# Optimization experiments

Measured on AMD Instinct MI355X. Metric: run time of the kernel, lower is better.

The kernel has to match this reference:

```python
import jax, jax.numpy as jnp
from jax import lax
import numpy as np

# ---- hyperparams (match init_kwargs) ----
NUM_HASHES = 8
BITS = 5
TABLE_SIZE = 64
M = 27            # ALSH augmentation length; M % (KH*KW) == 0
U = 0.83
KH = KW = 3
STRIDE = 1
PAD = 1
OUT_CHANNELS = 256
IN_CHANNELS = 64


def setup_inputs() -> dict:
    key = jax.random.key(0)
    k1, k2, k3 = jax.random.split(key, 3)
    x = jax.random.normal(k1, (32, IN_CHANNELS, 56, 56), jnp.float32)
    kernels = jax.random.normal(k2, (OUT_CHANNELS, IN_CHANNELS, KH, KW), jnp.float32) * 0.05
    a = jax.random.normal(k3, (NUM_HASHES * BITS, IN_CHANNELS * KH * KW + M), jnp.float32)
    return {"x": x, "kernels": kernels, "a": a}


def _scale_under_U(kv):
    # ScaleUnder_U: rescale all kernel vectors so max L2 norm == U
    norms = jnp.sqrt(jnp.sum(kv * kv, axis=1))
    return kv * (U / jnp.max(norms))


def _P(kv):
    # ALSH preprocessing: append ||x||^2, ||x||^4, ..., ||x||^(2^M)
    p = jnp.sum(kv * kv, axis=1, keepdims=True)  # ||x||^2
    cols = []
    for _ in range(M):
        cols.append(p)
        p = p * p
    return jnp.concatenate([kv] + cols, axis=1)  # [K, D+M]


_BIT_W = (2 ** jnp.arange(BITS)).astype(jnp.int32)


def _hash_vectors(a, v):
    # v: [K, D+M] -> bucket indices [NUM_HASHES, K]
    proj = v @ a.T                                   # [K, NUM_HASHES*BITS]
    bits = (proj > 0).astype(jnp.int32).reshape(-1, NUM_HASHES, BITS)
    idx = jnp.einsum('khb,b->hk', bits, _BIT_W)      # multi-bit SRP index
    return idx % TABLE_SIZE


def _build_table(bucket):
    # vectorized equivalent of the nested scalar-scatter loops in init_table:
    # append kernel id i to table[bucket[h, i]] in (h-major, i-minor) order.
    H, K = bucket.shape
    flat = bucket.reshape(-1)                        # [H*K]
    vals = (jnp.arange(H * K) % K).astype(jnp.int32) # stored value = kernel index i
    order = jnp.argsort(flat)                        # stable in jax
    sb, sv = flat[order], vals[order]
    pos = jnp.arange(H * K) - jnp.searchsorted(sb, sb, side='left')  # slot within bucket
    row_len = H * K
    table = jnp.zeros((TABLE_SIZE, row_len), jnp.int32).at[sb, pos].set(sv)
    lengths = jnp.zeros((TABLE_SIZE,), jnp.int32).at[flat].add(1)
    return table, lengths


def _vote_buckets(x, a):
    # Q: append M/(KH*KW) constant 1/2 planes; hash via convolution with a reshaped
    N, C, H, W = x.shape
    m_planes = M // (KH * KW)
    xq = jnp.concatenate([x, jnp.full((N, m_planes, H, W), 0.5, x.dtype)], axis=1)
    hk = a.reshape(NUM_HASHES * BITS, C + m_planes, KH, KW)  # a_to_kernel
    d = lax.conv_general_dilated(xq, hk, (STRIDE, STRIDE), [(PAD, PAD), (PAD, PAD)],
                                 dimension_numbers=('NCHW', 'OIHW', 'NCHW'))
    # [N, NUM_HASHES*BITS, H', W'] -> bucket per (hash fn, location)
    Np, _, Hp, Wp = d.shape
    bits = (d > 0).astype(jnp.int32).reshape(Np, NUM_HASHES, BITS, Hp * Wp)
    buckets = jnp.einsum('nhbs,b->hns', bits, _BIT_W) % TABLE_SIZE  # [H, N, S]
    return buckets.reshape(NUM_HASHES, -1)


def _active_mask(x, kernels, a):
    K = kernels.shape[0]
    kv = kernels.reshape(K, -1)
    buckets_k = _hash_vectors(a, _P(_scale_under_U(kv)))   # [H, K]
    table, lengths = _build_table(buckets_k)
    votes = _vote_buckets(x, a)                            # [H, N*S]
    tallied = jnp.zeros((NUM_HASHES, TABLE_SIZE), jnp.int32).at[
        jnp.arange(NUM_HASHES)[:, None], votes].add(1)     # count_votes
    indices = jnp.argmax(tallied, axis=1)                  # best bucket per hash fn
    entries = table[indices]                               # [H, row_len]
    valid = jnp.arange(table.shape[1])[None, :] < lengths[indices][:, None]
    # union of kernel ids across selected buckets (== sort+unique gather)
    mask = jnp.zeros((K,), jnp.float32).at[entries.reshape(-1)].max(
        valid.reshape(-1).astype(jnp.float32))
    return mask, tallied, indices


def reference(x, kernels, a):
    mask, tallied, indices = _active_mask(x, kernels, a)
    out = lax.conv_general_dilated(x, kernels, (STRIDE, STRIDE), [(PAD, PAD), (PAD, PAD)],
                                   dimension_numbers=('NCHW', 'OIHW', 'NCHW'))
    out = out * mask[None, :, None, None]  # conv restricted to the active kernel set
    return out, tallied, indices, mask
```

## Files before the change

### kernel.cpp

```cpp
#include <hip/hip_runtime.h>
#include <math.h>

#define NH 8
#define BITS_ 5
#define NB 40
#define TS 64
#define MAUG 27
#define CIN 64
#define HH 56
#define WW 56
#define NN 32
#define OCH 256
#define DK 576
#define DPM 603
#define HW (HH*WW)

#define UST 59
#define LO_OFF 7552
#define SMEM_DW 15104

typedef __attribute__((ext_vector_type(4))) float f32x4;
typedef __attribute__((ext_vector_type(8))) _Float16 f16x8;
typedef union { uint4 u; f16x8 h; } fragh_u;

__device__ __forceinline__ unsigned int f16b(float v) {
    union { _Float16 h; unsigned short u; } cv;
    cv.h = (_Float16)v;
    return (unsigned int)cv.u;
}
__device__ __forceinline__ float f16tof(unsigned int b) {
    union { _Float16 h; unsigned short u; } cv;
    cv.u = (unsigned short)b;
    return (float)cv.h;
}

__global__ void kP(const float* __restrict__ kern, const float* __restrict__ a,
                   float* __restrict__ aT, float* __restrict__ ctab,
                   int* __restrict__ tallied, float* __restrict__ normP,
                   unsigned short* __restrict__ whA,
                   unsigned short* __restrict__ vaH, unsigned short* __restrict__ vaL)
{
    const int bid = blockIdx.x;
    const int t = threadIdx.x;
    if (bid < 32) {
        for (int idx = bid * 256 + t; idx < DPM * NB; idx += 32 * 256) {
            int d = idx / NB, j = idx - d * NB;
            aT[idx] = a[j * DPM + d];
        }
    } else if (bid == 32) {
        for (int g = t; g < 9 * NB; g += 256) {
            int pat = g / NB, j = g - pat * NB;
            int ry = pat / 3, rx = pat % 3;
            float s = 0.f;
            for (int ky = 0; ky < 3; ++ky) {
                if (ry == 0 && ky == 0) continue;
                if (ry == 2 && ky == 2) continue;
                for (int kx = 0; kx < 3; ++kx) {
                    if (rx == 0 && kx == 0) continue;
                    if (rx == 2 && kx == 2) continue;
                    for (int mc = 0; mc < 3; ++mc)
                        s += a[j * DPM + DK + mc * 9 + ky * 3 + kx];
                }
            }
            ctab[g] = 0.5f * s;
        }
        for (int g = t; g < NH * TS; g += 256) tallied[g] = 0;
    } else if (bid < 37) {
        int g = (bid - 33) * 256 + t;
        int oc = g >> 2, part = g & 3;
        const float4* p = (const float4*)(kern + oc * DK + part * 144);
        float sq = 0.f;
        #pragma unroll 4
        for (int i = 0; i < 36; ++i) {
            float4 v = p[i];
            sq += v.x * v.x + v.y * v.y + v.z * v.z + v.w * v.w;
        }
        normP[g] = sq;
    } else {
        int idx = (bid - 37) * 256 + t;
        int f = idx >> 6, lane = idx & 63;
        if (f < 288) {
            const int kidxG = f >> 4, mf = f & 15;
            const int tap = kidxG % 9, cc = kidxG / 9;
            const int oc = mf * 16 + (lane & 15);
            const int cbase = cc * 32 + (lane >> 4) * 8;
            unsigned int hs[8];
            #pragma unroll
            for (int j = 0; j < 8; ++j)
                hs[j] = f16b(kern[oc * DK + (cbase + j) * 9 + tap]);
            unsigned int* p = (unsigned int*)(whA + ((size_t)f * 64 + lane) * 8);
            #pragma unroll
            for (int w2 = 0; w2 < 4; ++w2)
                p[w2] = hs[2 * w2] | (hs[2 * w2 + 1] << 16);
        } else if (f < 342) {
            const int fv = f - 288;
            const int kidxG = fv / 3, mfv = fv % 3;
            const int tap = kidxG % 9, cc = kidxG / 9;
            const int j = mfv * 16 + (lane & 15);
            const int cbase = cc * 32 + (lane >> 4) * 8;
            unsigned int hs[8], ls[8];
            #pragma unroll
            for (int jj = 0; jj < 8; ++jj) {
                float w = (j < NB) ? a[j * DPM + (cbase + jj) * 9 + tap] : 0.f;
                unsigned int h = f16b(w);
                unsigned int l = f16b(w - f16tof(h));
                hs[jj] = h; ls[jj] = l;
            }
            unsigned int* ph = (unsigned int*)(vaH + ((size_t)fv * 64 + lane) * 8);
            unsigned int* pl = (unsigned int*)(vaL + ((size_t)fv * 64 + lane) * 8);
            #pragma unroll
            for (int w2 = 0; w2 < 4; ++w2) {
                ph[w2] = hs[2 * w2] | (hs[2 * w2 + 1] << 16);
                pl[w2] = ls[2 * w2] | (ls[2 * w2 + 1] << 16);
            }
        }
    }
}

__global__ void __launch_bounds__(256) kH(const float* __restrict__ kern,
        const float* __restrict__ aT, const float* __restrict__ normP,
        int* __restrict__ bucket_k)
{
    __shared__ float xs[DK];
    __shared__ float red[256];
    __shared__ float accR[3 * 41];
    __shared__ float proj[NB];
    const int t = threadIdx.x;
    const int lane = t & 63, ty = t >> 6;
    const int oc = blockIdx.x;

    red[t] = fmaxf(fmaxf(normP[t], normP[t + 256]), fmaxf(normP[t + 512], normP[t + 768]));
    __syncthreads();
    for (int s = 128; s > 0; s >>= 1) {
        if (t < s) red[t] = fmaxf(red[t], red[t + s]);
        __syncthreads();
    }
    const float scale = 0.83f / sqrtf(red[0]);
    for (int i = t; i < DK; i += 256) xs[i] = scale * kern[(size_t)oc * DK + i];
    __syncthreads();

    const int j = (lane < NB) ? lane : (NB - 1);
    float acc = 0.f, sq = 0.f;
    const int d0 = ty * 144;
    for (int d = d0; d < d0 + 144; ++d) {
        float xv = xs[d];
        sq += xv * xv;
        acc += xv * aT[d * NB + j];
    }
    if (ty > 0) {
        if (lane < NB) accR[(ty - 1) * 41 + lane] = acc;
        if (lane == NB) accR[(ty - 1) * 41 + 40] = sq;
    }
    __syncthreads();
    if (ty == 0 && lane < NB) {
        acc += (accR[lane] + accR[41 + lane]) + accR[82 + lane];
        sq += (accR[40] + accR[81]) + accR[122];
        float pv = sq;
        for (int m = 0; m < MAUG; ++m) {
            acc += pv * aT[(DK + m) * NB + lane];
            pv = pv * pv;
        }
        proj[lane] = acc;
    }
    __syncthreads();
    if (t < NH) {
        int b = 0;
        #pragma unroll
        for (int bb = 0; bb < BITS_; ++bb)
            if (proj[t * BITS_ + bb] > 0.f) b |= (1 << bb);
        bucket_k[t * OCH + oc] = b & (TS - 1);
    }
}

#define ADX(kidx, nb) ((rowu + ((((kidx) % 9) / 3) * 8 + ((kidx) / 9) * 4) * UST + (nb) + (((kidx) % 9) % 3)) * 4)

__global__ void __launch_bounds__(512, 4) kM(const float* __restrict__ x,
        const unsigned short* __restrict__ whA,
        const unsigned short* __restrict__ vaH, const unsigned short* __restrict__ vaL,
        const float* __restrict__ ctab, int* __restrict__ tallied,
        float* __restrict__ out)
{
    __shared__ unsigned int smem[SMEM_DW];
    const int lane = threadIdx.x, wid = threadIdx.y;
    const int y0 = blockIdx.x * 2, n = blockIdx.y;
    const int lcol = lane & 15, hi4 = lane >> 4;
    const int t = wid * 64 + lane;
    const int mg = wid & 3, ng = wid >> 2;
    const int colbase = (mg == 3) ? 40 : mg * 16;
    const uint4* wbase = (const uint4*)whA + (size_t)mg * 4 * 64 + lane;
    const int rowu = (ng * 8 + hi4) * UST + lcol;

    fragh_u ahA[4], ahB[4];
    #pragma unroll
    for (int mf = 0; mf < 4; ++mf) ahA[mf].u = wbase[mf * 64];

    {
        const int r = wid & 3, half = wid >> 2;
        const int y = y0 - 1 + r;
        const bool valid = (lane < WW) && (y >= 0) && (y < HH);
        const int colc = (lane < WW) ? lane : (WW - 1);
        const int yc = (y >= 0 && y < HH) ? y : 0;
        const float* xb = x + (((size_t)n * CIN + half * 32) * HH + yc) * WW + colc;
        float xv[32];
        #pragma unroll
        for (int i = 0; i < 32; ++i) xv[i] = xb[(size_t)i * HW];

        if (t < 256) {
            const int tile = t >> 7, rem = t & 127;
            const int L = (rem & 1) ? 57 : 0;
            const int u = (rem >> 1) & 7, rr = rem >> 4;
            *(uint4*)&smem[tile * LO_OFF + ((rr * 8 + u) * UST + L) * 4] =
                make_uint4(0u, 0u, 0u, 0u);
        }

        #pragma unroll
        for (int uu = 0; uu < 4; ++uu) {
            unsigned int dh[4], dl[4];
            #pragma unroll
            for (int dd = 0; dd < 4; ++dd) {
                float v0 = valid ? xv[uu * 8 + dd * 2] : 0.f;
                float v1 = valid ? xv[uu * 8 + dd * 2 + 1] : 0.f;
                unsigned int h0 = f16b(v0), h1 = f16b(v1);
                unsigned int l0 = f16b(v0 - f16tof(h0));
                unsigned int l1 = f16b(v1 - f16tof(h1));
                dh[dd] = h0 | (h1 << 16);
                dl[dd] = l0 | (l1 << 16);
            }
            if (lane < WW) {
                const int ad = ((r * 8 + half * 4 + uu) * UST + 1 + lane) * 4;
                *(uint4*)&smem[ad] = make_uint4(dh[0], dh[1], dh[2], dh[3]);
                *(uint4*)&smem[LO_OFF + ad] = make_uint4(dl[0], dl[1], dl[2], dl[3]);
            }
        }
    }
    __syncthreads();

    {
        f32x4 acc[4][4];
        #pragma unroll
        for (int mf = 0; mf < 4; ++mf)
            #pragma unroll
            for (int nf = 0; nf < 4; ++nf)
                acc[mf][nf] = (f32x4){0.f, 0.f, 0.f, 0.f};

        fragh_u bhP[3];
        bhP[0].u = *(const uint4*)&smem[ADX(0, 0)];
        bhP[1].u = *(const uint4*)&smem[ADX(0, 16)];

        #pragma unroll
        for (int step = 0; step < 72; ++step) {
            const int kidx = step >> 2, nf = step & 3;
            fragh_u* cur = (kidx & 1) ? ahB : ahA;
            fragh_u* nxt = (kidx & 1) ? ahA : ahB;
            if (nf == 0 && kidx < 17) {
                #pragma unroll
                for (int mf = 0; mf < 4; ++mf)
                    nxt[mf].u = wbase[(kidx + 1) * 1024 + mf * 64];
            }
            if (step + 2 < 72) {
                const int s2 = step + 2;
                const int k2 = s2 >> 2, nf2 = s2 & 3;
                const int nb2 = (nf2 == 3) ? 40 : nf2 * 16;
                bhP[s2 % 3].u = *(const uint4*)&smem[ADX(k2, nb2)];
            }
            const fragh_u bh = bhP[step % 3];
            acc[0][nf] = __builtin_amdgcn_mfma_f32_16x16x32_f16(cur[0].h, bh.h, acc[0][nf], 0, 0, 0);
            acc[1][nf] = __builtin_amdgcn_mfma_f32_16x16x32_f16(cur[1].h, bh.h, acc[1][nf], 0, 0, 0);
            acc[2][nf] = __builtin_amdgcn_mfma_f32_16x16x32_f16(cur[2].h, bh.h, acc[2][nf], 0, 0, 0);
            acc[3][nf] = __builtin_amdgcn_mfma_f32_16x16x32_f16(cur[3].h, bh.h, acc[3][nf], 0, 0, 0);
        }

        const int yrow = y0 + ng;
        #pragma unroll
        for (int mf = 0; mf < 4; ++mf) {
            #pragma unroll
            for (int reg = 0; reg < 4; ++reg) {
                const int oc = (mg * 4 + mf) * 16 + hi4 * 4 + reg;
                float* ob = out + (((size_t)n * OCH + oc) * HH + yrow) * WW;
                #pragma unroll
                for (int nf = 0; nf < 4; ++nf) {
                    const int col = ((nf == 3) ? 40 : nf * 16) + lcol;
                    ob[col] = acc[mf][nf][reg];
                }
            }
        }
    }

    f32x4 vacc[3];
    vacc[0] = (f32x4){0.f, 0.f, 0.f, 0.f};
    vacc[1] = (f32x4){0.f, 0.f, 0.f, 0.f};
    vacc[2] = (f32x4){0.f, 0.f, 0.f, 0.f};
    {
        const uint4* vbH = (const uint4*)vaH + lane;
        const uint4* vbL = (const uint4*)vaL + lane;
        fragh_u vh[3], vl[3];
        fragh_u bhV[2], blV[2];
        vh[0].u = vbH[0];   vl[0].u = vbL[0];
        vh[1].u = vbH[64];  vl[1].u = vbL[64];
        bhV[0].u = *(const uint4*)&smem[ADX(0, colbase)];
        blV[0].u = *(const uint4*)&smem[LO_OFF + ADX(0, colbase)];
        #pragma unroll
        for (int s = 0; s < 54; ++s) {
            const int kidx = s / 3, mfv = s % 3;
            const int b = kidx & 1;
            if (s + 2 < 54) {
                vh[(s + 2) % 3].u = vbH[(s + 2) * 64];
                vl[(s + 2) % 3].u = vbL[(s + 2) * 64];
            }
            if (mfv == 0 && kidx < 17) {
                bhV[b ^ 1].u = *(const uint4*)&smem[ADX(kidx + 1, colbase)];
                blV[b ^ 1].u = *(const uint4*)&smem[LO_OFF + ADX(kidx + 1, colbase)];
            }
            const fragh_u vhc = vh[s % 3], vlc = vl[s % 3];
            vacc[mfv] = __builtin_amdgcn_mfma_f32_16x16x32_f16(vhc.h, bhV[b].h, vacc[mfv], 0, 0, 0);
            vacc[mfv] = __builtin_amdgcn_mfma_f32_16x16x32_f16(vhc.h, blV[b].h, vacc[mfv], 0, 0, 0);
            vacc[mfv] = __builtin_amdgcn_mfma_f32_16x16x32_f16(vlc.h, bhV[b].h, vacc[mfv], 0, 0, 0);
        }
    }

    __syncthreads();
    float* projT = (float*)smem;
    int* hist = (int*)&smem[6144];
    {
        const int px = colbase + lcol;
        #pragma unroll
        for (int mfv = 0; mfv < 3; ++mfv)
            #pragma unroll
            for (int reg = 0; reg < 4; ++reg)
                projT[(ng * 64 + px) * 49 + mfv * 16 + hi4 * 4 + reg] = vacc[mfv][reg];
    }
    hist[t] = 0;
    __syncthreads();
    if (t < 2 * WW) {
        const int row = t / WW, pxx = t - row * WW;
        const int yv = y0 + row;
        const int ry = (yv == 0) ? 0 : ((yv == HH - 1) ? 2 : 1);
        const int rx = (pxx == 0) ? 0 : ((pxx == WW - 1) ? 2 : 1);
        const float* ct = ctab + (ry * 3 + rx) * NB;
        const float* pr = projT + (row * 64 + pxx) * 49;
        #pragma unroll
        for (int h = 0; h < NH; ++h) {
            int b = 0;
            #pragma unroll
            for (int bb = 0; bb < BITS_; ++bb)
                if (pr[h * BITS_ + bb] + ct[h * BITS_ + bb] > 0.f) b |= (1 << bb);
            atomicAdd(&hist[h * TS + (b & (TS - 1))], 1);
        }
    }
    __syncthreads();
    {
        int v = hist[t];
        if (v) atomicAdd(&tallied[t], v);
    }
}

__global__ void kC(const int* __restrict__ tallied, const int* __restrict__ bucket_k,
                   float* __restrict__ o_tallied, float* __restrict__ o_indices,
                   float* __restrict__ o_mask, int* __restrict__ mask_i)
{
    const int t = threadIdx.x;
    __shared__ int s_idx[NH];
    if (t < NH) {
        int best = tallied[t * TS];
        int bi = 0;
        for (int b = 1; b < TS; ++b) {
            int v = tallied[t * TS + b];
            if (v > best) { best = v; bi = b; }
        }
        s_idx[t] = bi;
        o_indices[t] = (float)bi;
    }
    for (int i = t; i < NH * TS; i += 256) o_tallied[i] = (float)tallied[i];
    __syncthreads();
    int mk = 0;
    #pragma unroll
    for (int hp = 0; hp < NH; ++hp) {
        int b = bucket_k[hp * OCH + t];
        #pragma unroll
        for (int h = 0; h < NH; ++h) mk |= (b == s_idx[h]) ? 1 : 0;
    }
    mask_i[t] = mk;
    o_mask[t] = (float)mk;
}

__global__ void __launch_bounds__(256) kZ(float* __restrict__ out,
                                          const int* __restrict__ mask_i)
{
    const int b = blockIdx.x;
    const int oc = b & (OCH - 1);
    if (mask_i[oc]) return;
    const int n = b >> 8;
    float4* o = (float4*)(out + ((size_t)n * OCH + oc) * HW);
    for (int i = threadIdx.x; i < HW / 4; i += 256)
        o[i] = make_float4(0.f, 0.f, 0.f, 0.f);
}

extern "C" void kernel_launch(void* const* d_in, const int* in_sizes, int n_in,
                              void* d_out, int out_size, void* d_ws, size_t ws_size,
                              hipStream_t stream)
{
    const float* x    = (const float*)d_in[0];
    const float* kern = (const float*)d_in[1];
    const float* a    = (const float*)d_in[2];

    float* out       = (float*)d_out;
    float* o_tallied = out + (size_t)NN * OCH * HW;
    float* o_indices = o_tallied + NH * TS;
    float* o_mask    = o_indices + NH;

    float* ws = (float*)d_ws;
    float* aT       = ws;
    float* ctab     = ws + 24320;
    float* normP    = ws + 24704;
    int*   tallied  = (int*)(ws + 25728);
    int*   bucket_k = (int*)(ws + 26240);
    int*   mask_i   = (int*)(ws + 28288);
    unsigned short* whA = (unsigned short*)(ws + 28544);
    unsigned short* vaH = (unsigned short*)(ws + 102272);
    unsigned short* vaL = (unsigned short*)(ws + 116096);

    kP<<<123, 256, 0, stream>>>(kern, a, aT, ctab, tallied, normP, whA, vaH, vaL);
    kH<<<OCH, 256, 0, stream>>>(kern, aT, normP, bucket_k);
    kM<<<dim3(28, NN), dim3(64, 8), 0, stream>>>(x, whA, vaH, vaL, ctab, tallied, out);
    kC<<<1, 256, 0, stream>>>(tallied, bucket_k, o_tallied, o_indices, o_mask, mask_i);
    kZ<<<NN * OCH, 256, 0, stream>>>(out, mask_i);
}
```

Baseline: 109.4 us.

## Fuse mask and zeroing kernels, swizzle conv block order, raise MFMA priority

Merges the single-block argmax/mask kernel into the zeroing kernel, so every block recomputes the per-hash argmax with a warp-shuffle reduction and its own mask bit. This removes one launch and the serial dependency on a one-block kernel. The main conv kernel also remaps block IDs with a swizzle so consecutive blocks spread across batch images, and it wraps its MFMA groups in s_setprio to favour matrix issue. Costs are redundant argmax work in every block and a different tie-breaking path in the shuffle reduction.

```diff
diff --git a/kernel.cpp b/kernel.cpp
--- a/kernel.cpp
+++ b/kernel.cpp
@@ -182,7 +182,10 @@
 {
     __shared__ unsigned int smem[SMEM_DW];
     const int lane = threadIdx.x, wid = threadIdx.y;
-    const int y0 = blockIdx.x * 2, n = blockIdx.y;
+    const int id = blockIdx.y * 28 + blockIdx.x;
+    const int swz = (id & 7) * 112 + (id >> 3);
+    const int n = swz / 28;
+    const int y0 = (swz - n * 28) * 2;
     const int lcol = lane & 15, hi4 = lane >> 4;
     const int t = wid * 64 + lane;
     const int mg = wid & 3, ng = wid >> 2;
@@ -264,10 +267,12 @@
                 bhP[s2 % 3].u = *(const uint4*)&smem[ADX(k2, nb2)];
             }
             const fragh_u bh = bhP[step % 3];
+            __builtin_amdgcn_s_setprio(1);
             acc[0][nf] = __builtin_amdgcn_mfma_f32_16x16x32_f16(cur[0].h, bh.h, acc[0][nf], 0, 0, 0);
             acc[1][nf] = __builtin_amdgcn_mfma_f32_16x16x32_f16(cur[1].h, bh.h, acc[1][nf], 0, 0, 0);
             acc[2][nf] = __builtin_amdgcn_mfma_f32_16x16x32_f16(cur[2].h, bh.h, acc[2][nf], 0, 0, 0);
             acc[3][nf] = __builtin_amdgcn_mfma_f32_16x16x32_f16(cur[3].h, bh.h, acc[3][nf], 0, 0, 0);
+            __builtin_amdgcn_s_setprio(0);
         }
 
         const int yrow = y0 + ng;
@@ -312,9 +317,11 @@
                 blV[b ^ 1].u = *(const uint4*)&smem[LO_OFF + ADX(kidx + 1, colbase)];
             }
             const fragh_u vhc = vh[s % 3], vlc = vl[s % 3];
+            __builtin_amdgcn_s_setprio(1);
             vacc[mfv] = __builtin_amdgcn_mfma_f32_16x16x32_f16(vhc.h, bhV[b].h, vacc[mfv], 0, 0, 0);
             vacc[mfv] = __builtin_amdgcn_mfma_f32_16x16x32_f16(vhc.h, blV[b].h, vacc[mfv], 0, 0, 0);
             vacc[mfv] = __builtin_amdgcn_mfma_f32_16x16x32_f16(vlc.h, bhV[b].h, vacc[mfv], 0, 0, 0);
+            __builtin_amdgcn_s_setprio(0);
         }
     }
 
@@ -354,44 +361,58 @@
     }
 }
 
-__global__ void kC(const int* __restrict__ tallied, const int* __restrict__ bucket_k,
-                   float* __restrict__ o_tallied, float* __restrict__ o_indices,
-                   float* __restrict__ o_mask, int* __restrict__ mask_i)
+__global__ void __launch_bounds__(256) kCZ(const int* __restrict__ tallied,
+        const int* __restrict__ bucket_k, float* __restrict__ o_tallied,
+        float* __restrict__ o_indices, float* __restrict__ o_mask,
+        float* __restrict__ out)
 {
+    __shared__ int s_idx[NH];
+    __shared__ int s_mk;
     const int t = threadIdx.x;
-    __shared__ int s_idx[NH];
-    if (t < NH) {
-        int best = tallied[t * TS];
-        int bi = 0;
-        for (int b = 1; b < TS; ++b) {
-            int v = tallied[t * TS + b];
-            if (v > best) { best = v; bi = b; }
-        }
-        s_idx[t] = bi;
-        o_indices[t] = (float)bi;
-    }
-    for (int i = t; i < NH * TS; i += 256) o_tallied[i] = (float)tallied[i];
-    __syncthreads();
-    int mk = 0;
-    #pragma unroll
-    for (int hp = 0; hp < NH; ++hp) {
-        int b = bucket_k[hp * OCH + t];
-        #pragma unroll
-        for (int h = 0; h < NH; ++h) mk |= (b == s_idx[h]) ? 1 : 0;
-    }
-    mask_i[t] = mk;
-    o_mask[t] = (float)mk;
-}
-
-__global__ void __launch_bounds__(256) kZ(float* __restrict__ out,
-                                          const int* __restrict__ mask_i)
-{
-    const int b = blockIdx.x;
-    const int oc = b & (OCH - 1);
-    if (mask_i[oc]) return;
-    const int n = b >> 8;
+    {
+        const int h = t >> 5, j = t & 31;
+        int v1 = tallied[h * TS + j], v2 = tallied[h * TS + 32 + j];
+        int v, idx;
+        if (v2 > v1) { v = v2; idx = 32 + j; } else { v = v1; idx = j; }
+        #pragma unroll
+        for (int s = 16; s > 0; s >>= 1) {
+            int ov = __shfl_down(v, s, 32);
+            int oi = __shfl_down(idx, s, 32);
+            if (ov > v || (ov == v && oi < idx)) { v = ov; idx = oi; }
+        }
+        if (j == 0) s_idx[h] = idx;
+    }
+    __syncthreads();
+    const int oc = blockIdx.x & (OCH - 1);
+    const int n = blockIdx.x >> 8;
+    if (t == 0) {
+        int mk = 0;
+        #pragma unroll
+        for (int hp = 0; hp < NH; ++hp) {
+            int b = bucket_k[hp * OCH + oc];
+            #pragma unroll
+            for (int h = 0; h < NH; ++h) mk |= (b == s_idx[h]) ? 1 : 0;
+        }
+        s_mk = mk;
+    }
+    if (blockIdx.x == 0) {
+        for (int i = t; i < NH * TS; i += 256) o_tallied[i] = (float)tallied[i];
+        if (t < NH) o_indices[t] = (float)s_idx[t];
+        {
+            int mk = 0;
+            #pragma unroll
+            for (int hp = 0; hp < NH; ++hp) {
+                int b = bucket_k[hp * OCH + t];
+                #pragma unroll
+                for (int h = 0; h < NH; ++h) mk |= (b == s_idx[h]) ? 1 : 0;
+            }
+            o_mask[t] = (float)mk;
+        }
+    }
+    __syncthreads();
+    if (s_mk) return;
     float4* o = (float4*)(out + ((size_t)n * OCH + oc) * HW);
-    for (int i = threadIdx.x; i < HW / 4; i += 256)
+    for (int i = t; i < HW / 4; i += 256)
         o[i] = make_float4(0.f, 0.f, 0.f, 0.f);
 }
 
@@ -414,7 +435,6 @@
     float* normP    = ws + 24704;
     int*   tallied  = (int*)(ws + 25728);
     int*   bucket_k = (int*)(ws + 26240);
-    int*   mask_i   = (int*)(ws + 28288);
     unsigned short* whA = (unsigned short*)(ws + 28544);
     unsigned short* vaH = (unsigned short*)(ws + 102272);
     unsigned short* vaL = (unsigned short*)(ws + 116096);
@@ -422,6 +442,5 @@
     kP<<<123, 256, 0, stream>>>(kern, a, aT, ctab, tallied, normP, whA, vaH, vaL);
     kH<<<OCH, 256, 0, stream>>>(kern, aT, normP, bucket_k);
     kM<<<dim3(28, NN), dim3(64, 8), 0, stream>>>(x, whA, vaH, vaL, ctab, tallied, out);
-    kC<<<1, 256, 0, stream>>>(tallied, bucket_k, o_tallied, o_indices, o_mask, mask_i);
-    kZ<<<NN * OCH, 256, 0, stream>>>(out, mask_i);
-}
+    kCZ<<<NN * OCH, 256, 0, stream>>>(tallied, bucket_k, o_tallied, o_indices, o_mask, out);
+}
```

Measured after the change: 105.1 us. -3.9%, faster.
